# Optimization experiments

Measured on AMD Instinct MI355X. Metric: run time of the kernel, lower is better.

## Reference

```python
import jax, jax.numpy as jnp
import numpy as np

MAX_DELTAS = 4
PACK = 8  # 4-bit values packed into int32
HIDDEN = 4096
Q_SLICE = 4096   # num_heads(32) * head_size(128)
KV_SLICE = 1024  # num_kv_heads(8) * head_size(128)
TOKENS = 4096


def setup_inputs() -> dict:
    key = jax.random.key(0)
    ks = jax.random.split(key, 16)
    imax = 2**31 - 1
    inp = {
        "x": jax.random.normal(ks[0], (TOKENS, HIDDEN), dtype=jnp.float32),
        "base_weight": jax.random.normal(ks[1], (Q_SLICE + 2 * KV_SLICE, HIDDEN), dtype=jnp.float32) * 0.02,
        "qweight_q": jax.random.randint(ks[2], (MAX_DELTAS, 1, HIDDEN // PACK, Q_SLICE), 0, imax, dtype=jnp.int32),
        "qweight_k": jax.random.randint(ks[3], (MAX_DELTAS, 1, HIDDEN // PACK, KV_SLICE), 0, imax, dtype=jnp.int32),
        "qweight_v": jax.random.randint(ks[4], (MAX_DELTAS, 1, HIDDEN // PACK, KV_SLICE), 0, imax, dtype=jnp.int32),
        "qzeros_q": jax.random.randint(ks[5], (MAX_DELTAS, 1, 1, Q_SLICE // PACK), 0, imax, dtype=jnp.int32),
        "qzeros_k": jax.random.randint(ks[6], (MAX_DELTAS, 1, 1, KV_SLICE // PACK), 0, imax, dtype=jnp.int32),
        "qzeros_v": jax.random.randint(ks[7], (MAX_DELTAS, 1, 1, KV_SLICE // PACK), 0, imax, dtype=jnp.int32),
        "scales_q": jax.random.uniform(ks[8], (MAX_DELTAS, 1, 1, Q_SLICE), dtype=jnp.float32) * 0.01,
        "scales_k": jax.random.uniform(ks[9], (MAX_DELTAS, 1, 1, KV_SLICE), dtype=jnp.float32) * 0.01,
        "scales_v": jax.random.uniform(ks[10], (MAX_DELTAS, 1, 1, KV_SLICE), dtype=jnp.float32) * 0.01,
        "indices": jax.random.randint(ks[11], (TOKENS,), 0, MAX_DELTAS, dtype=jnp.int32),
    }
    return inp


def _unpack_rows(qw):
    # (D, 1, K//PACK, N) int32 -> (D, K, N) 4-bit values, packed along K
    D, _, Kp, N = qw.shape
    shifts = (jnp.arange(PACK, dtype=jnp.int32) * 4)
    q = (qw[:, 0, :, None, :] >> shifts[None, None, :, None]) & 0xF  # (D,Kp,PACK,N)
    return q.reshape(D, Kp * PACK, N)


def _unpack_cols(qz):
    # (D, 1, 1, N//PACK) int32 -> (D, N), packed along N
    D = qz.shape[0]
    shifts = (jnp.arange(PACK, dtype=jnp.int32) * 4)
    z = (qz[:, 0, 0, :, None] >> shifts[None, None, :]) & 0xF  # (D, N//PACK, PACK)
    return z.reshape(D, -1)


def _dequant(qw, qz, sc):
    # GPTQ-style dequant, single group (g_idx is all zeros): W = (q - (z+1)) * scale
    q = _unpack_rows(qw).astype(jnp.float32)            # (D, K, N)
    z = (_unpack_cols(qz) + 1).astype(jnp.float32)      # (D, N)
    return (q - z[:, None, :]) * sc[:, 0, 0, :][:, None, :]


def _delta_slice(x, indices, qw, qz, sc):
    # per-token indexed delta matmul: out[t] = x[t] @ W[indices[t]] (0 if index==-1)
    W = _dequant(qw, qz, sc)  # (D, K, N)
    out = jnp.zeros((x.shape[0], W.shape[2]), dtype=x.dtype)
    for d in range(MAX_DELTAS):
        mask = (indices == d).astype(x.dtype)[:, None]
        out = out + (x * mask) @ W[d]
    return out


def reference(x, base_weight, qweight_q, qweight_k, qweight_v,
              qzeros_q, qzeros_k, qzeros_v,
              scales_q, scales_k, scales_v, indices):
    # base merged QKV projection
    base_out = x @ base_weight.T  # (T, q + 2*kv)
    # per-slice delta adds (offsets handled by concatenation order: q, k, v)
    dq = _delta_slice(x, indices, qweight_q, qzeros_q, scales_q)
    dk = _delta_slice(x, indices, qweight_k, qzeros_k, scales_k)
    dv = _delta_slice(x, indices, qweight_v, qzeros_v, scales_v)
    return base_out + jnp.concatenate([dq, dk, dv], axis=1)
```

## Files before the change

kernel.cpp:

```cpp
#include <hip/hip_runtime.h>
#include <stdint.h>

#define TOKENS 4096
#define HIDDEN 4096
#define NQ     4096
#define NKV    1024
#define NTOT   6144
#define KPACK  512
#define MAXTILES 20

typedef __attribute__((ext_vector_type(8))) __bf16 bf16x8;
typedef __attribute__((ext_vector_type(8))) short short8v;
typedef __attribute__((ext_vector_type(4))) float floatx4;

__device__ __forceinline__ short f2bf(float f) {
  union { float f; unsigned u; } v; v.f = f;
  unsigned r = v.u + 0x7fffu + ((v.u >> 16) & 1u);
  return (short)(r >> 16);
}

__device__ __forceinline__ void load_lds16(const void* g, void* l) {
  __builtin_amdgcn_global_load_lds((__attribute__((address_space(1))) void*)(g),
                                   (__attribute__((address_space(3))) void*)(l),
                                   16, 0, 0);
}

__global__ __launch_bounds__(256) void prep_tokens(const int* __restrict__ idx,
                                                   int* __restrict__ token_list,
                                                   int* __restrict__ grp) {
  __shared__ int cnt[4], cur[4];
  const int tid = threadIdx.x;
  if (tid < 4) cnt[tid] = 0;
  __syncthreads();
  for (int t = tid; t < TOKENS; t += 256) {
    int d = idx[t];
    if ((unsigned)d < 4u) atomicAdd(&cnt[d], 1);
  }
  __syncthreads();
  if (tid == 0) {
    int s = 0, nt = 0;
    for (int d = 0; d < 4; d++) {
      cur[d] = s; grp[d] = s; grp[4 + d] = cnt[d]; s += cnt[d];
      int tiles = (cnt[d] + 255) >> 8;
      for (int rt = 0; rt < tiles; rt++) grp[9 + nt++] = d | (rt << 2);
    }
    grp[8] = nt;
  }
  __syncthreads();
  for (int t = tid; t < TOKENS; t += 256) {
    int d = idx[t];
    if ((unsigned)d < 4u) {
      int p = atomicAdd(&cur[d], 1);
      token_list[p] = t;
    }
  }
}

__global__ __launch_bounds__(256) void cvt_x(const float* __restrict__ x,
                                             short* __restrict__ xb) {
  size_t g = (size_t)blockIdx.x * 256 + threadIdx.x;
  size_t i = g * 8;
  float4 a = ((const float4*)(x + i))[0];
  float4 b = ((const float4*)(x + i))[1];
  short8v o;
  o[0] = f2bf(a.x); o[1] = f2bf(a.y); o[2] = f2bf(a.z); o[3] = f2bf(a.w);
  o[4] = f2bf(b.x); o[5] = f2bf(b.y); o[6] = f2bf(b.z); o[7] = f2bf(b.w);
  *(short8v*)(xb + i) = o;
}

__global__ __launch_bounds__(256) void combine_w(
    const float* __restrict__ bw,
    const int* __restrict__ qwq, const int* __restrict__ qwk, const int* __restrict__ qwv,
    const int* __restrict__ qzq, const int* __restrict__ qzk, const int* __restrict__ qzv,
    const float* __restrict__ scq, const float* __restrict__ sck, const float* __restrict__ scv,
    short* __restrict__ wc) {
  __shared__ int ldsq[4][8][72];
  __shared__ float zs[4][64], ss[4][64];
  const int tid = threadIdx.x;
  const int n0  = blockIdx.y * 64;
  const int kp0 = blockIdx.x * 8;

  const int* qw; const int* qz; const float* sc; int Ns, nb;
  if (n0 < NQ)            { qw = qwq; qz = qzq; sc = scq; Ns = NQ;  nb = n0; }
  else if (n0 < NQ + NKV) { qw = qwk; qz = qzk; sc = sck; Ns = NKV; nb = n0 - NQ; }
  else                    { qw = qwv; qz = qzv; sc = scv; Ns = NKV; nb = n0 - NQ - NKV; }

  {
    int d = tid >> 6, n = tid & 63;
    int nn = nb + n;
    int z = (int)(((unsigned)qz[d * (Ns >> 3) + (nn >> 3)] >> ((nn & 7) * 4)) & 0xFu);
    zs[d][n] = (float)(z + 1);
    ss[d][n] = sc[d * Ns + nn];
  }

#pragma unroll
  for (int d = 0; d < 4; d++) {
#pragma unroll
    for (int p = 0; p < 2; p++) {
      int i  = tid + p * 256;
      int kp = i >> 6, n = i & 63;
      ldsq[d][kp][n] = qw[((size_t)d * KPACK + kp0 + kp) * Ns + nb + n];
    }
  }
  __syncthreads();

  const int kp = tid & 7;
#pragma unroll
  for (int p = 0; p < 2; p++) {
    int n = (tid >> 3) + p * 32;
    const float4* bp = (const float4*)(bw + (size_t)(n0 + n) * HIDDEN + (kp0 + kp) * 8);
    float4 b0 = bp[0], b1 = bp[1];
    float bv[8] = {b0.x, b0.y, b0.z, b0.w, b1.x, b1.y, b1.z, b1.w};
#pragma unroll
    for (int d = 0; d < 4; d++) {
      unsigned q32 = (unsigned)ldsq[d][kp][n];
      float z = zs[d][n], s = ss[d][n];
      short8v o;
#pragma unroll
      for (int j = 0; j < 8; j++)
        o[j] = f2bf(((float)((q32 >> (4 * j)) & 0xFu) - z) * s + bv[j]);
      *(short8v*)(wc + ((size_t)d * NTOT + n0 + n) * HIDDEN + (kp0 + kp) * 8) = o;
    }
  }
}

__device__ __forceinline__ void rdB(const short* Bb, int wn, int mrow, int sx,
                                    bf16x8 bf[4]) {
#pragma unroll
  for (int j = 0; j < 4; j++)
    bf[j] = *(const bf16x8*)(Bb + (wn * 64 + j * 16 + mrow) * 32 + sx);
}
__device__ __forceinline__ void rdA(const short* Ab, int wm, int g, int mrow,
                                    int sx, bf16x8 af[4]) {
#pragma unroll
  for (int i = 0; i < 4; i++)
    af[i] = *(const bf16x8*)(Ab + (wm * 128 + (g * 4 + i) * 16 + mrow) * 32 + sx);
}
__device__ __forceinline__ void mm(const bf16x8 af[4], const bf16x8 bf[4],
                                   floatx4 acc[8][4], int g) {
  __builtin_amdgcn_s_setprio(1);
#pragma unroll
  for (int i = 0; i < 4; i++)
#pragma unroll
    for (int j = 0; j < 4; j++)
      acc[g * 4 + i][j] =
          __builtin_amdgcn_mfma_f32_16x16x32_bf16(af[i], bf[j], acc[g * 4 + i][j], 0, 0, 0);
  __builtin_amdgcn_s_setprio(0);
}
__device__ __forceinline__ void st2(short* dst, const short* g0, const short* g1,
                                    int ko) {
  load_lds16(g0 + ko, dst);
  load_lds16(g1 + ko, dst + 512);
}

#define BARRIER __builtin_amdgcn_s_barrier()
#define LGKM0 asm volatile("s_waitcnt lgkmcnt(0)" ::: "memory")
#define VMC4  asm volatile("s_waitcnt vmcnt(4)" ::: "memory")
#define VMC0  asm volatile("s_waitcnt vmcnt(0)" ::: "memory")

#define PH_O(RB, RA, SD, KO)                                   \
  rdB(RB, wn, mrow, sx, bf);                                   \
  rdA(RA, wm, 0, mrow, sx, af);                                \
  st2((SD) + wave * 1024, gA0, gA1, (KO));                     \
  BARRIER; LGKM0; mm(af, bf, acc, 0); BARRIER;
#define PH_E(RA, SD, KO)                                       \
  rdA(RA, wm, 1, mrow, sx, af);                                \
  st2((SD) + wave * 1024, gB0, gB1, (KO));                     \
  VMC4; BARRIER; LGKM0; mm(af, bf, acc, 1); BARRIER;

__global__ __launch_bounds__(512, 2) void gemm_grouped(
    const short* __restrict__ xb, const short* __restrict__ wc,
    const int* __restrict__ token_list, const int* __restrict__ grp,
    float* __restrict__ out) {
  const int nt = grp[8];
  if ((int)blockIdx.y >= nt) return;
  const int te = grp[9 + blockIdx.y];
  const int d  = te & 3;
  const int rt = te >> 2;
  const int cnt   = grp[4 + d];
  const int start = grp[d];
  const int n0 = blockIdx.x * 256;

  __shared__ __align__(16) short Ak[2][2][8192];
  __shared__ __align__(16) short Bk[2][2][8192];
  __shared__ int toks[256];

  const int tid = threadIdx.x;
  if (tid < 256) {
    int r = rt * 256 + tid;
    if (r >= cnt) r = cnt - 1;
    toks[tid] = token_list[start + r];
  }
  __syncthreads();

  const int wave = tid >> 6;
  const int lane = tid & 63;

  const int sw = ((lane & 3) ^ ((lane >> 3) & 3)) * 8;

  const int arow = wave * 32 + (lane >> 2);
  const short* gA0 = xb + (size_t)toks[arow] * HIDDEN + sw;
  const short* gA1 = xb + (size_t)toks[arow + 16] * HIDDEN + sw;
  const short* wrow = wc + ((size_t)d * NTOT + n0) * HIDDEN;
  const short* gB0 = wrow + (size_t)arow * HIDDEN + sw;
  const short* gB1 = gB0 + (size_t)16 * HIDDEN;

  const int mrow = lane & 15;
  const int sx = (((lane >> 4) ^ ((mrow >> 1) & 3))) * 8;
  const int wm = wave >> 2;
  const int wn = wave & 3;

  floatx4 acc[8][4];
#pragma unroll
  for (int i = 0; i < 8; i++)
#pragma unroll
    for (int j = 0; j < 4; j++) acc[i][j] = (floatx4){0.f, 0.f, 0.f, 0.f};

  bf16x8 af[4], bf[4];

  st2(&Ak[0][0][0] + wave * 1024, gA0, gA1, 0);
  st2(&Bk[0][0][0] + wave * 1024, gB0, gB1, 0);
  st2(&Ak[0][1][0] + wave * 1024, gA0, gA1, 32);
  st2(&Bk[0][1][0] + wave * 1024, gB0, gB1, 32);
  VMC4;
  BARRIER;

  for (int it = 0; it < 31; ++it) {
    const int kb = it * 128;
    PH_O(&Bk[0][0][0], &Ak[0][0][0], &Ak[1][0][0], kb + 64);
    PH_E(&Ak[0][0][0],               &Bk[1][0][0], kb + 64);
    PH_O(&Bk[0][1][0], &Ak[0][1][0], &Ak[1][1][0], kb + 96);
    PH_E(&Ak[0][1][0],               &Bk[1][1][0], kb + 96);
    PH_O(&Bk[1][0][0], &Ak[1][0][0], &Ak[0][0][0], kb + 128);
    PH_E(&Ak[1][0][0],               &Bk[0][0][0], kb + 128);
    PH_O(&Bk[1][1][0], &Ak[1][1][0], &Ak[0][1][0], kb + 160);
    PH_E(&Ak[1][1][0],               &Bk[0][1][0], kb + 160);
  }
  PH_O(&Bk[0][0][0], &Ak[0][0][0], &Ak[1][0][0], 4032);
  PH_E(&Ak[0][0][0],               &Bk[1][0][0], 4032);
  PH_O(&Bk[0][1][0], &Ak[0][1][0], &Ak[1][1][0], 4064);
  PH_E(&Ak[0][1][0],               &Bk[1][1][0], 4064);
  rdB(&Bk[1][0][0], wn, mrow, sx, bf);
  rdA(&Ak[1][0][0], wm, 0, mrow, sx, af);
  BARRIER; LGKM0; mm(af, bf, acc, 0); BARRIER;
  rdA(&Ak[1][0][0], wm, 1, mrow, sx, af);
  VMC0; BARRIER; LGKM0; mm(af, bf, acc, 1); BARRIER;
  rdB(&Bk[1][1][0], wn, mrow, sx, bf);
  rdA(&Ak[1][1][0], wm, 0, mrow, sx, af);
  BARRIER; LGKM0; mm(af, bf, acc, 0); BARRIER;
  rdA(&Ak[1][1][0], wm, 1, mrow, sx, af);
  BARRIER; LGKM0; mm(af, bf, acc, 1);

  const int rbase = (lane >> 4) * 4;
  const int coll  = lane & 15;
#pragma unroll
  for (int i = 0; i < 8; i++) {
#pragma unroll
    for (int r = 0; r < 4; r++) {
      int m = wm * 128 + i * 16 + rbase + r;
      if (rt * 256 + m < cnt) {
        float* orow = out + (size_t)toks[m] * NTOT + n0 + wn * 64 + coll;
#pragma unroll
        for (int j = 0; j < 4; j++) orow[j * 16] = acc[i][j][r];
      }
    }
  }
}

extern "C" void kernel_launch(void* const* d_in, const int* in_sizes, int n_in,
                              void* d_out, int out_size, void* d_ws, size_t ws_size,
                              hipStream_t stream) {
  const float* x   = (const float*)d_in[0];
  const float* bw  = (const float*)d_in[1];
  const int*   qwq = (const int*)d_in[2];
  const int*   qwk = (const int*)d_in[3];
  const int*   qwv = (const int*)d_in[4];
  const int*   qzq = (const int*)d_in[5];
  const int*   qzk = (const int*)d_in[6];
  const int*   qzv = (const int*)d_in[7];
  const float* scq = (const float*)d_in[8];
  const float* sck = (const float*)d_in[9];
  const float* scv = (const float*)d_in[10];
  const int*   idx = (const int*)d_in[11];
  float* out = (float*)d_out;

  char* ws = (char*)d_ws;
  short* xb = (short*)ws;
  short* wc = (short*)(ws + (size_t)33554432);
  int* token_list = (int*)(ws + (size_t)33554432 + 201326592);
  int* grp = token_list + TOKENS;

  prep_tokens<<<1, 256, 0, stream>>>(idx, token_list, grp);
  cvt_x<<<(TOKENS * HIDDEN) / (256 * 8), 256, 0, stream>>>(x, xb);
  dim3 gc(HIDDEN / 64, NTOT / 64);
  combine_w<<<gc, 256, 0, stream>>>(bw, qwq, qwk, qwv, qzq, qzk, qzv, scq, sck, scv, wc);
  dim3 gg(NTOT / 256, MAXTILES);
  gemm_grouped<<<gg, 512, 0, stream>>>(xb, wc, token_list, grp, out);
}
```

Baseline: 572.1 us.

## Remap GEMM workgroups for XCD-aware L2 locality and prefetch base weights early

The grouped GEMM now linearizes its 2D grid and remaps the workgroup index so that consecutive logical tiles (same token group, adjacent N tiles) land on the same XCD. This should improve L2 reuse of the shared A rows and weight tiles across the 8 XCDs of MI355X. The combine_w kernel also issues its base-weight float4 loads before the packed-weight LDS staging and barrier, so that global latency overlaps. The remap assumes the grid x dimension is exactly 24 and adds integer division per block.

After: 585.8 us. 2.4% more time.

```diff
diff --git a/kernel.cpp b/kernel.cpp
--- a/kernel.cpp
+++ b/kernel.cpp
@@ -85,6 +85,16 @@
   else if (n0 < NQ + NKV) { qw = qwk; qz = qzk; sc = sck; Ns = NKV; nb = n0 - NQ; }
   else                    { qw = qwv; qz = qzv; sc = scv; Ns = NKV; nb = n0 - NQ - NKV; }
 
+  const int kp = tid & 7;
+
+  float4 c00, c01, c10, c11;
+  {
+    int na = (tid >> 3), nb2 = (tid >> 3) + 32;
+    const float4* bp0 = (const float4*)(bw + (size_t)(n0 + na) * HIDDEN + (kp0 + kp) * 8);
+    const float4* bp1 = (const float4*)(bw + (size_t)(n0 + nb2) * HIDDEN + (kp0 + kp) * 8);
+    c00 = bp0[0]; c01 = bp0[1]; c10 = bp1[0]; c11 = bp1[1];
+  }
+
   {
     int d = tid >> 6, n = tid & 63;
     int nn = nb + n;
@@ -98,18 +108,17 @@
 #pragma unroll
     for (int p = 0; p < 2; p++) {
       int i  = tid + p * 256;
-      int kp = i >> 6, n = i & 63;
-      ldsq[d][kp][n] = qw[((size_t)d * KPACK + kp0 + kp) * Ns + nb + n];
-    }
-  }
-  __syncthreads();
-
-  const int kp = tid & 7;
+      int kpp = i >> 6, n = i & 63;
+      ldsq[d][kpp][n] = qw[((size_t)d * KPACK + kp0 + kpp) * Ns + nb + n];
+    }
+  }
+  __syncthreads();
+
 #pragma unroll
   for (int p = 0; p < 2; p++) {
     int n = (tid >> 3) + p * 32;
-    const float4* bp = (const float4*)(bw + (size_t)(n0 + n) * HIDDEN + (kp0 + kp) * 8);
-    float4 b0 = bp[0], b1 = bp[1];
+    float4 b0 = p ? c10 : c00;
+    float4 b1 = p ? c11 : c01;
     float bv[8] = {b0.x, b0.y, b0.z, b0.w, b1.x, b1.y, b1.z, b1.w};
 #pragma unroll
     for (int d = 0; d < 4; d++) {
@@ -173,13 +182,17 @@
     const int* __restrict__ token_list, const int* __restrict__ grp,
     float* __restrict__ out) {
   const int nt = grp[8];
-  if ((int)blockIdx.y >= nt) return;
-  const int te = grp[9 + blockIdx.y];
+  const int nwg = nt * 24;
+  const int orig = (int)blockIdx.y * 24 + (int)blockIdx.x;
+  if (orig >= nwg) return;
+  const int q = nwg >> 3, r = nwg & 7, xcd = orig & 7;
+  const int w = (xcd < r ? xcd * (q + 1) : r * (q + 1) + (xcd - r) * q) + (orig >> 3);
+  const int te = grp[9 + w / 24];
   const int d  = te & 3;
   const int rt = te >> 2;
   const int cnt   = grp[4 + d];
   const int start = grp[d];
-  const int n0 = blockIdx.x * 256;
+  const int n0 = (w % 24) * 256;
 
   __shared__ __align__(16) short Ak[2][2][8192];
   __shared__ __align__(16) short Bk[2][2][8192];
@@ -187,9 +200,9 @@
 
   const int tid = threadIdx.x;
   if (tid < 256) {
-    int r = rt * 256 + tid;
-    if (r >= cnt) r = cnt - 1;
-    toks[tid] = token_list[start + r];
+    int rr = rt * 256 + tid;
+    if (rr >= cnt) rr = cnt - 1;
+    toks[tid] = token_list[start + rr];
   }
   __syncthreads();
 
@@ -256,12 +269,12 @@
 #pragma unroll
   for (int i = 0; i < 8; i++) {
 #pragma unroll
-    for (int r = 0; r < 4; r++) {
-      int m = wm * 128 + i * 16 + rbase + r;
+    for (int rr = 0; rr < 4; rr++) {
+      int m = wm * 128 + i * 16 + rbase + rr;
       if (rt * 256 + m < cnt) {
         float* orow = out + (size_t)toks[m] * NTOT + n0 + wn * 64 + coll;
 #pragma unroll
-        for (int j = 0; j < 4; j++) orow[j * 16] = acc[i][j][r];
+        for (int j = 0; j < 4; j++) orow[j * 16] = acc[i][j][rr];
       }
     }
   }
```
